# Kernel tuning notes

Measured on AMD Instinct MI355X. Metric: run time of the kernel, lower is better.

The kernel has to match this reference:

```python
import jax, jax.numpy as jnp
import numpy as np

F_DIM = 32          # phi_feature_dim
P = 128             # preselection_ap (spatial H=W)
NU = 4              # num_users
N1 = NU - 1         # n_cat1 == n_cat2
N3 = (NU - 1) ** 2  # n_cat3


def setup_inputs() -> dict:
    key = jax.random.key(0)
    k1, k2, k3, k4, k5 = jax.random.split(key, 5)
    B, CIN = 32, 8
    phi_input = jax.random.normal(k1, (B, CIN, P, P), dtype=jnp.float32)
    W1 = jax.random.normal(k2, (4 * F_DIM, CIN), dtype=jnp.float32) * 0.1
    b1 = jax.random.normal(k3, (4 * F_DIM,), dtype=jnp.float32) * 0.1
    W3 = jax.random.normal(k4, (4 * F_DIM, 4 * F_DIM), dtype=jnp.float32) * 0.1
    b3 = jax.random.normal(k5, (4 * F_DIM,), dtype=jnp.float32) * 0.1
    ex = jnp.ones((P, P), dtype=jnp.float32) - jnp.eye(P, dtype=jnp.float32)
    return {"phi_input": phi_input, "W1": W1, "b1": b1, "W3": W3, "b3": b3, "ex": ex}


def _conv1x1(x, W, b):
    # 1x1 conv == channel matmul: [b,c,h,w] x [o,c] -> [b,o,h,w]
    return jnp.einsum('bchw,oc->bohw', x, W) + b[None, :, None, None]


def _postprocess(r, ex):
    f = F_DIM
    c0 = r[:, :f]
    c1 = jnp.einsum('ph,bchw->bcpw', ex, r[:, f:2 * f]) / N1
    c2 = jnp.einsum('bchw,wq->bchq', r[:, 2 * f:3 * f], ex) / N1
    c3 = jnp.einsum('ph,bchw,wq->bcpq', ex, r[:, 3 * f:4 * f], ex) / N3
    return jnp.concatenate((c0, c1, c2, c3), axis=1)


def reference(phi_input, W1, b1, W3, b3, ex):
    r = jax.nn.relu(_conv1x1(phi_input, W1, b1))
    r = _postprocess(r, ex)
    r = jax.nn.relu(_conv1x1(r, W3, b3))
    r = _postprocess(r, ex)
    return r
```

## Files before the change

### kernel.cpp

```cpp
#include <hip/hip_runtime.h>
#include <stdint.h>

#define BATCH 32
#define CIN   8
#define NCH   128
#define PP    128
#define VCH   96
#define NSTRIP 8

typedef __attribute__((ext_vector_type(8))) short    bf16x8;
typedef __attribute__((ext_vector_type(4))) float    f32x4;

__device__ __forceinline__ float bf2f(unsigned short u) {
    union { unsigned int i; float f; } x; x.i = ((unsigned int)u) << 16; return x.f;
}
__device__ __forceinline__ unsigned short f2bf(float f) {
    union { float f; unsigned int i; } x; x.f = f;
    unsigned int r = x.i + 0x7fffu + ((x.i >> 16) & 1u);
    return (unsigned short)(r >> 16);
}
__device__ __forceinline__ unsigned int pk2(float a, float b) {
    return (unsigned int)f2bf(a) | ((unsigned int)f2bf(b) << 16);
}

#define SWZB(row, cb) (((row) << 8) + ((cb) ^ (((row) & 7) << 4)))

__global__ __launch_bounds__(512) void k1_sums(const float* __restrict__ phi,
        const float* __restrict__ W1, const float* __restrict__ b1,
        float* __restrict__ RS1t, float* __restrict__ CS1p) {
    __shared__ float S[17408];
    int bx = blockIdx.x;
    int b = bx >> 3, strip = bx & 7;
    int p0 = strip * 16;
    int tid = threadIdx.x;
    int c = tid & 127, qq = tid >> 7;

    #pragma unroll
    for (int i = 0; i < 8; ++i) {
        int idx = tid + i * 512;
        int pi = idx >> 8, ci = (idx >> 5) & 7, q4 = (idx & 31) * 4;
        float4 v = *(const float4*)(phi + ((size_t)(b * CIN + ci) * PP + p0 + pi) * PP + q4);
        *(float4*)(S + pi * 1024 + ci * 128 + q4) = v;
    }
    float4 w1a = *(const float4*)(W1 + c * 8);
    float4 w1b = *(const float4*)(W1 + c * 8 + 4);
    float b1c = b1[c];
    float cs_acc[32];
    #pragma unroll
    for (int j = 0; j < 32; ++j) cs_acc[j] = 0.f;
    float rsp[16];
    __syncthreads();

    for (int pi = 0; pi < 16; ++pi) {
        float rs = 0.f;
        const float* pb = S + pi * 1024;
        #pragma unroll
        for (int j4 = 0; j4 < 8; ++j4) {
            int q4 = qq * 32 + j4 * 4;
            float4 ph[8];
            #pragma unroll
            for (int ci = 0; ci < 8; ++ci)
                ph[ci] = *(const float4*)(pb + ci * 128 + q4);
            #pragma unroll
            for (int e = 0; e < 4; ++e) {
                float t = b1c;
                t = fmaf(w1a.x, ((const float*)&ph[0])[e], t);
                t = fmaf(w1a.y, ((const float*)&ph[1])[e], t);
                t = fmaf(w1a.z, ((const float*)&ph[2])[e], t);
                t = fmaf(w1a.w, ((const float*)&ph[3])[e], t);
                t = fmaf(w1b.x, ((const float*)&ph[4])[e], t);
                t = fmaf(w1b.y, ((const float*)&ph[5])[e], t);
                t = fmaf(w1b.z, ((const float*)&ph[6])[e], t);
                t = fmaf(w1b.w, ((const float*)&ph[7])[e], t);
                t = fmaxf(t, 0.f);
                cs_acc[j4 * 4 + e] += t;
                rs += t;
            }
        }
        rsp[pi] = rs;
    }
    __syncthreads();
    #pragma unroll
    for (int pi = 0; pi < 16; ++pi) S[pi * 512 + tid] = rsp[pi];
    __syncthreads();
    #pragma unroll
    for (int i = 0; i < 4; ++i) {
        int idx = tid + i * 512;
        int pi = idx >> 7, cc = idx & 127;
        float s = S[pi * 512 + cc] + S[pi * 512 + 128 + cc]
                + S[pi * 512 + 256 + cc] + S[pi * 512 + 384 + cc];
        RS1t[((size_t)b * PP + p0 + pi) * NCH + cc] = s;
    }
    __syncthreads();
    #pragma unroll
    for (int j4 = 0; j4 < 8; ++j4) {
        float4 v = {cs_acc[j4 * 4], cs_acc[j4 * 4 + 1], cs_acc[j4 * 4 + 2], cs_acc[j4 * 4 + 3]};
        *(float4*)(S + c * 132 + qq * 32 + j4 * 4) = v;
    }
    __syncthreads();
    float* dstp = CS1p + (size_t)(b * NSTRIP + strip) * NCH * PP;
    for (int k = tid; k < 16384; k += 512) {
        int cc = k >> 7, q = k & 127;
        dstp[k] = S[cc * 132 + q];
    }
}

__global__ __launch_bounds__(256) void k1b_planes(const float* __restrict__ W3,
        const float* __restrict__ b3, const float* __restrict__ RS1t,
        const float* __restrict__ CS1p, float* __restrict__ Ap,
        float* __restrict__ Bqt, unsigned short* __restrict__ W3bf) {
    int bx = blockIdx.x;
    int b = bx >> 2, og = bx & 3;
    int tid = threadIdx.x;
    __shared__ float cs_g[64][132];
    __shared__ float rs_g[64][132];
    __shared__ float s1_96[32];
    for (int k = tid; k < 64 * 128; k += 256) {
        int r = k >> 7, q = k & 127;
        int ch_c = (r < 32) ? (32 + r) : (64 + r);
        float s = 0.f;
        #pragma unroll
        for (int s8 = 0; s8 < NSTRIP; ++s8)
            s += CS1p[((size_t)(b * NSTRIP + s8) * NCH + ch_c) * PP + q];
        cs_g[r][q] = s;
    }
    for (int k = tid; k < 64 * 128; k += 256) {
        int p = k >> 6, r = k & 63;
        rs_g[r][p] = RS1t[((size_t)b * PP + p) * NCH + 64 + r];
    }
    __syncthreads();
    if (tid < 32) {
        float s = 0.f;
        for (int q = 0; q < 128; ++q) s += cs_g[32 + tid][q];
        s1_96[tid] = s;
    }
    int o = og * 32 + (tid >> 3), qh = tid & 7;
    {
        float wa[64];
        #pragma unroll
        for (int r = 0; r < 64; ++r)
            wa[r] = (r < 32) ? W3[o * NCH + 32 + r] * (1.f / 3.f)
                             : -W3[o * NCH + 64 + r] * (1.f / 9.f);
        #pragma unroll
        for (int j = 0; j < 4; ++j) {
            int q = qh * 16 + j * 4;
            float4 a = {0.f, 0.f, 0.f, 0.f};
            #pragma unroll
            for (int r = 0; r < 64; ++r) {
                float4 cv = *(const float4*)&cs_g[r][q];
                a.x = fmaf(wa[r], cv.x, a.x);
                a.y = fmaf(wa[r], cv.y, a.y);
                a.z = fmaf(wa[r], cv.z, a.z);
                a.w = fmaf(wa[r], cv.w, a.w);
            }
            *(float4*)&Ap[((size_t)b * NCH + o) * PP + q] = a;
        }
    }
    __syncthreads();
    float cc = b3[o];
    #pragma unroll
    for (int r = 0; r < 32; ++r)
        cc = fmaf(W3[o * NCH + 96 + r] * (1.f / 9.f), s1_96[r], cc);
    {
        float wb[64];
        #pragma unroll
        for (int r = 0; r < 64; ++r)
            wb[r] = (r < 32) ? W3[o * NCH + 64 + r] * (1.f / 3.f)
                             : -W3[o * NCH + 64 + r] * (1.f / 9.f);
        #pragma unroll
        for (int j = 0; j < 4; ++j) {
            int p4 = qh * 16 + j * 4;
            float4 a = {0.f, 0.f, 0.f, 0.f};
            #pragma unroll
            for (int r = 0; r < 64; ++r) {
                float4 rv = *(const float4*)&rs_g[r][p4];
                a.x = fmaf(wb[r], rv.x, a.x);
                a.y = fmaf(wb[r], rv.y, a.y);
                a.z = fmaf(wb[r], rv.z, a.z);
                a.w = fmaf(wb[r], rv.w, a.w);
            }
            Bqt[((size_t)b * PP + p4 + 0) * NCH + o] = a.x + cc;
            Bqt[((size_t)b * PP + p4 + 1) * NCH + o] = a.y + cc;
            Bqt[((size_t)b * PP + p4 + 2) * NCH + o] = a.z + cc;
            Bqt[((size_t)b * PP + p4 + 3) * NCH + o] = a.w + cc;
        }
    }
    if (bx == 0) {
        for (int i = 0; i < 16; ++i) {
            int k = tid + i * 256;
            float4 w = *(const float4*)(W3 + k * 4);
            int c0 = (k * 4) & 127;
            float sc = (c0 < 32) ? 1.f : ((c0 < 96) ? (-1.f / 3.f) : (1.f / 9.f));
            unsigned int lo = pk2(w.x * sc, w.y * sc);
            unsigned int hi = pk2(w.z * sc, w.w * sc);
            uint2 u = {lo, hi};
            *(uint2*)(W3bf + k * 4) = u;
        }
    }
}

__global__ __launch_bounds__(512, 4) void k2_mfma(const float* __restrict__ phi,
        const float* __restrict__ W1, const float* __restrict__ b1,
        const unsigned short* __restrict__ W3bf,
        const float* __restrict__ Ap, const float* __restrict__ Bqt,
        float* __restrict__ out, unsigned short* __restrict__ v2) {
    int bx = blockIdx.x;
    int b = bx >> 4, strip = bx & 15;
    int p0 = strip * 8;
    __shared__ unsigned short w3_l[16384];
    __shared__ unsigned short t_l[16384];
    __shared__ unsigned short phi_b[2][1024];
    __shared__ float BC_l[2][128];
    int tid = threadIdx.x;
    int wv = tid >> 6, l = tid & 63, lr = l & 15, lg = l >> 4;

    #pragma unroll
    for (int i = 0; i < 4; ++i) {
        int k = tid + i * 512;
        int o = k >> 4, cb = (k & 15) * 16;
        bf16x8 v = *(const bf16x8*)(W3bf + k * 8);
        *(bf16x8*)((char*)w3_l + SWZB(o, cb)) = v;
    }
    bf16x8 w1fr = {0, 0, 0, 0, 0, 0, 0, 0};
    if (lg == 0) {
        int cc = wv * 16 + lr;
        float4 wa = *(const float4*)(W1 + cc * 8);
        float4 wb = *(const float4*)(W1 + cc * 8 + 4);
        w1fr[0] = (short)f2bf(wa.x); w1fr[1] = (short)f2bf(wa.y);
        w1fr[2] = (short)f2bf(wa.z); w1fr[3] = (short)f2bf(wa.w);
        w1fr[4] = (short)f2bf(wb.x); w1fr[5] = (short)f2bf(wb.y);
        w1fr[6] = (short)f2bf(wb.z); w1fr[7] = (short)f2bf(wb.w);
    }
    int c0 = wv * 16 + lg * 4;
    f32x4 binit = {b1[c0], b1[c0 + 1], b1[c0 + 2], b1[c0 + 3]};
    if (tid < 128) {
        int q = tid;
        bf16x8 pv;
        #pragma unroll
        for (int ci = 0; ci < 8; ++ci)
            pv[ci] = (short)f2bf(phi[((size_t)(b * CIN + ci) * PP + p0) * PP + q]);
        *(bf16x8*)(phi_b[0] + q * 8) = pv;
        BC_l[0][tid] = Bqt[((size_t)b * PP + p0) * NCH + tid];
    }
    __syncthreads();

    for (int r = 0; r < 8; ++r) {
        int cur = r & 1, nxt = cur ^ 1;
        int p = p0 + r;
        float pfv[8]; float bcn = 0.f;
        if (r < 7 && tid < 128) {
            int q = tid;
            #pragma unroll
            for (int ci = 0; ci < 8; ++ci)
                pfv[ci] = phi[((size_t)(b * CIN + ci) * PP + p + 1) * PP + q];
            bcn = Bqt[((size_t)b * PP + p + 1) * NCH + tid];
        }
        const unsigned short* pb = phi_b[cur];
        #pragma unroll
        for (int pt = 0; pt < 8; ++pt) {
            int pix = pt * 16 + lr;
            bf16x8 bfr1 = {0, 0, 0, 0, 0, 0, 0, 0};
            if (lg == 0) bfr1 = *(const bf16x8*)(pb + pix * 8);
            f32x4 a = __builtin_amdgcn_mfma_f32_16x16x32_bf16(w1fr, bfr1, binit, 0, 0, 0);
            uint2 u;
            u.x = pk2(fmaxf(a.x, 0.f), fmaxf(a.y, 0.f));
            u.y = pk2(fmaxf(a.z, 0.f), fmaxf(a.w, 0.f));
            *(uint2*)((char*)t_l + SWZB(pix, c0 * 2)) = u;
        }
        __syncthreads();
        bf16x8 afr[4];
        #pragma unroll
        for (int ks = 0; ks < 4; ++ks)
            afr[ks] = *(const bf16x8*)((char*)t_l + SWZB(wv * 16 + lr, ks * 64 + lg * 16));
        f32x4 acc[8];
        #pragma unroll
        for (int nt = 0; nt < 8; ++nt) {
            int o = nt * 16 + lr;
            f32x4 ap = *(const f32x4*)(Ap + ((size_t)(b * NCH + o)) * PP + wv * 16 + lg * 4);
            acc[nt] = ap + BC_l[cur][o];
        }
        #pragma unroll
        for (int nt = 0; nt < 8; ++nt) {
            int o = nt * 16 + lr;
            bf16x8 bfr[4];
            #pragma unroll
            for (int ks = 0; ks < 4; ++ks)
                bfr[ks] = *(const bf16x8*)((char*)w3_l + SWZB(o, ks * 64 + lg * 16));
            #pragma unroll
            for (int ks = 0; ks < 4; ++ks)
                acc[nt] = __builtin_amdgcn_mfma_f32_16x16x32_bf16(afr[ks], bfr[ks], acc[nt], 0, 0, 0);
        }
        __syncthreads();
        #pragma unroll
        for (int nt = 0; nt < 2; ++nt) {
            int o = nt * 16 + lr;
            f32x4 a = acc[nt];
            f32x4 rr = {fmaxf(a.x, 0.f), fmaxf(a.y, 0.f), fmaxf(a.z, 0.f), fmaxf(a.w, 0.f)};
            *(f32x4*)(out + ((size_t)(b * NCH + o) * PP + p) * PP + wv * 16 + lg * 4) = rr;
        }
        #pragma unroll
        for (int nt = 2; nt < 8; ++nt) {
            int o = nt * 16 + lr;
            f32x4 a = acc[nt];
            uint2 u;
            u.x = pk2(fmaxf(a.x, 0.f), fmaxf(a.y, 0.f));
            u.y = pk2(fmaxf(a.z, 0.f), fmaxf(a.w, 0.f));
            *(uint2*)((char*)t_l + SWZB(o, (wv * 16 + lg * 4) * 2)) = u;
        }
        if (r < 7 && tid < 128) {
            bf16x8 pv;
            #pragma unroll
            for (int ci = 0; ci < 8; ++ci) pv[ci] = (short)f2bf(pfv[ci]);
            *(bf16x8*)(phi_b[nxt] + tid * 8) = pv;
            BC_l[nxt][tid] = bcn;
        }
        __syncthreads();
        #pragma unroll
        for (int i = 0; i < 3; ++i) {
            int k = tid + i * 512;
            int o = 32 + (k >> 4), j = k & 15;
            bf16x8 v = *(const bf16x8*)((char*)t_l + SWZB(o, j * 16));
            *(bf16x8*)(v2 + ((size_t)(b * VCH + (o - 32)) * PP + p) * PP + j * 8) = v;
        }
        __syncthreads();
    }
}

__global__ __launch_bounds__(256) void k3_out(const unsigned short* __restrict__ v2,
        float* __restrict__ out) {
    int bx = blockIdx.x;
    int b = bx / VCH, cr = bx - b * VCH;
    int ch = 32 + cr;
    int g = ch >> 5;
    __shared__ float rsp[128][16];
    __shared__ float csp[16][128];
    __shared__ float rs_l[128], cs_l[128];
    __shared__ float s_sh;
    int tid = threadIdx.x;
    const unsigned short* src = v2 + (size_t)(b * VCH + cr) * (PP * PP);

    int pc = tid >> 4, qc = tid & 15;
    float cs8[8];
    #pragma unroll
    for (int e = 0; e < 8; ++e) cs8[e] = 0.f;
    #pragma unroll
    for (int i = 0; i < 8; ++i) {
        int pr = pc * 8 + i;
        bf16x8 u = *(const bf16x8*)(src + pr * PP + qc * 8);
        float rp = 0.f;
        #pragma unroll
        for (int e = 0; e < 8; ++e) {
            float v = bf2f((unsigned short)u[e]);
            cs8[e] += v;
            rp += v;
        }
        rsp[pr][qc] = rp;
    }
    f32x4 clo = {cs8[0], cs8[1], cs8[2], cs8[3]};
    f32x4 chi = {cs8[4], cs8[5], cs8[6], cs8[7]};
    *(f32x4*)&csp[pc][qc * 8]     = clo;
    *(f32x4*)&csp[pc][qc * 8 + 4] = chi;
    __syncthreads();
    if (tid < 128) {
        f32x4 a  = *(const f32x4*)&rsp[tid][0];
        f32x4 c2 = *(const f32x4*)&rsp[tid][4];
        f32x4 c3 = *(const f32x4*)&rsp[tid][8];
        f32x4 c4 = *(const f32x4*)&rsp[tid][12];
        rs_l[tid] = (a.x + a.y + a.z + a.w) + (c2.x + c2.y + c2.z + c2.w)
                  + (c3.x + c3.y + c3.z + c3.w) + (c4.x + c4.y + c4.z + c4.w);
    } else {
        int q = tid - 128;
        float s = 0.f;
        #pragma unroll
        for (int i = 0; i < 16; ++i) s += csp[i][q];
        cs_l[q] = s;
    }
    __syncthreads();
    if (tid < 64) {
        float s = rs_l[tid] + rs_l[tid + 64];
        #pragma unroll
        for (int off = 32; off > 0; off >>= 1) s += __shfl_down(s, off);
        if (tid == 0) s_sh = s;
    }
    __syncthreads();
    float stot = s_sh;

    float* dst = out + (size_t)(b * NCH + ch) * (PP * PP);
    #pragma unroll
    for (int i = 0; i < 8; ++i) {
        int k = tid + i * 256;
        int pr = k >> 4, q0 = (k & 15) * 8;
        bf16x8 u = *(const bf16x8*)(src + pr * PP + q0);
        float rp = rs_l[pr];
        float o8[8];
        #pragma unroll
        for (int e = 0; e < 8; ++e) {
            float v = bf2f((unsigned short)u[e]);
            float cq = cs_l[q0 + e];
            float r;
            if (g == 1)      r = (cq - v) * (1.f / 3.f);
            else if (g == 2) r = (rp - v) * (1.f / 3.f);
            else             r = (stot - rp - cq + v) * (1.f / 9.f);
            o8[e] = r;
        }
        f32x4 lo = {o8[0], o8[1], o8[2], o8[3]};
        f32x4 hi = {o8[4], o8[5], o8[6], o8[7]};
        *(f32x4*)(dst + pr * PP + q0)     = lo;
        *(f32x4*)(dst + pr * PP + q0 + 4) = hi;
    }
}

extern "C" void kernel_launch(void* const* d_in, const int* in_sizes, int n_in,
                              void* d_out, int out_size, void* d_ws, size_t ws_size,
                              hipStream_t stream) {
    (void)in_sizes; (void)n_in; (void)out_size; (void)ws_size;
    const float* phi = (const float*)d_in[0];
    const float* W1  = (const float*)d_in[1];
    const float* b1  = (const float*)d_in[2];
    const float* W3  = (const float*)d_in[3];
    const float* b3  = (const float*)d_in[4];
    float* out = (float*)d_out;

    char* ws = (char*)d_ws;
    unsigned short* v2 = (unsigned short*)ws;
    size_t off = (size_t)BATCH * VCH * PP * PP * 2;
    float* RS1t = (float*)(ws + off); off += (size_t)BATCH * NCH * PP * 4;
    float* CS1p = (float*)(ws + off); off += (size_t)BATCH * NSTRIP * NCH * PP * 4;
    float* Ap   = (float*)(ws + off); off += (size_t)BATCH * NCH * PP * 4;
    float* Bqt  = (float*)(ws + off); off += (size_t)BATCH * NCH * PP * 4;
    unsigned short* W3bf = (unsigned short*)(ws + off); off += (size_t)NCH * NCH * 2;

    k1_sums<<<BATCH * NSTRIP, 512, 0, stream>>>(phi, W1, b1, RS1t, CS1p);
    k1b_planes<<<BATCH * 4, 256, 0, stream>>>(W3, b3, RS1t, CS1p, Ap, Bqt, W3bf);
    k2_mfma<<<BATCH * 16, 512, 0, stream>>>(phi, W1, b1, W3bf, Ap, Bqt, out, v2);
    k3_out<<<BATCH * VCH, 256, 0, stream>>>(v2, out);
}
```

Before: 207.4 us.

## Recompute second-stage activations instead of storing bf16 intermediate and re-reading it

The second-layer MFMA pass now runs twice. A first pass computes only the row and column sums needed by the second postprocess, and a small kernel reduces the per-strip column partials. A final pass recomputes the activations and writes the finished output directly. This removes the large bf16 v2 intermediate write and read and the separate k3 pass. In exchange the conv and MFMA work is roughly doubled and one more kernel launch is added.

```diff
diff --git a/kernel.cpp b/kernel.cpp
--- a/kernel.cpp
+++ b/kernel.cpp
@@ -5,8 +5,8 @@
 #define CIN   8
 #define NCH   128
 #define PP    128
-#define VCH   96
 #define NSTRIP 8
+#define KSTRIP 16
 
 typedef __attribute__((ext_vector_type(8))) short    bf16x8;
 typedef __attribute__((ext_vector_type(4))) float    f32x4;
@@ -199,11 +199,11 @@
     }
 }
 
-__global__ __launch_bounds__(512, 4) void k2_mfma(const float* __restrict__ phi,
+__global__ __launch_bounds__(512, 4) void k2a_sums(const float* __restrict__ phi,
         const float* __restrict__ W1, const float* __restrict__ b1,
         const unsigned short* __restrict__ W3bf,
         const float* __restrict__ Ap, const float* __restrict__ Bqt,
-        float* __restrict__ out, unsigned short* __restrict__ v2) {
+        float* __restrict__ RSvT, float* __restrict__ CSp) {
     int bx = blockIdx.x;
     int b = bx >> 4, strip = bx & 15;
     int p0 = strip * 8;
@@ -211,8 +211,10 @@
     __shared__ unsigned short t_l[16384];
     __shared__ unsigned short phi_b[2][1024];
     __shared__ float BC_l[2][128];
+    __shared__ float rs_part[8][64];
     int tid = threadIdx.x;
     int wv = tid >> 6, l = tid & 63, lr = l & 15, lg = l >> 4;
+    int q0 = wv * 16 + lg * 4;
 
     #pragma unroll
     for (int i = 0; i < 4; ++i) {
@@ -234,25 +236,27 @@
     int c0 = wv * 16 + lg * 4;
     f32x4 binit = {b1[c0], b1[c0 + 1], b1[c0 + 2], b1[c0 + 3]};
     if (tid < 128) {
-        int q = tid;
         bf16x8 pv;
         #pragma unroll
         for (int ci = 0; ci < 8; ++ci)
-            pv[ci] = (short)f2bf(phi[((size_t)(b * CIN + ci) * PP + p0) * PP + q]);
-        *(bf16x8*)(phi_b[0] + q * 8) = pv;
+            pv[ci] = (short)f2bf(phi[((size_t)(b * CIN + ci) * PP + p0) * PP + tid]);
+        *(bf16x8*)(phi_b[0] + tid * 8) = pv;
         BC_l[0][tid] = Bqt[((size_t)b * PP + p0) * NCH + tid];
     }
     __syncthreads();
+
+    f32x4 cs_acc[4];
+    #pragma unroll
+    for (int i = 0; i < 4; ++i) { f32x4 z = {0.f, 0.f, 0.f, 0.f}; cs_acc[i] = z; }
 
     for (int r = 0; r < 8; ++r) {
         int cur = r & 1, nxt = cur ^ 1;
         int p = p0 + r;
         float pfv[8]; float bcn = 0.f;
         if (r < 7 && tid < 128) {
-            int q = tid;
             #pragma unroll
             for (int ci = 0; ci < 8; ++ci)
-                pfv[ci] = phi[((size_t)(b * CIN + ci) * PP + p + 1) * PP + q];
+                pfv[ci] = phi[((size_t)(b * CIN + ci) * PP + p + 1) * PP + tid];
             bcn = Bqt[((size_t)b * PP + p + 1) * NCH + tid];
         }
         const unsigned short* pb = phi_b[cur];
@@ -272,13 +276,153 @@
         #pragma unroll
         for (int ks = 0; ks < 4; ++ks)
             afr[ks] = *(const bf16x8*)((char*)t_l + SWZB(wv * 16 + lr, ks * 64 + lg * 16));
-        f32x4 acc[8];
-        #pragma unroll
-        for (int nt = 0; nt < 8; ++nt) {
+        #pragma unroll
+        for (int nt = 2; nt < 8; ++nt) {
             int o = nt * 16 + lr;
-            f32x4 ap = *(const f32x4*)(Ap + ((size_t)(b * NCH + o)) * PP + wv * 16 + lg * 4);
-            acc[nt] = ap + BC_l[cur][o];
-        }
+            bf16x8 bfr[4];
+            #pragma unroll
+            for (int ks = 0; ks < 4; ++ks)
+                bfr[ks] = *(const bf16x8*)((char*)w3_l + SWZB(o, ks * 64 + lg * 16));
+            f32x4 ap = *(const f32x4*)(Ap + ((size_t)(b * NCH + o)) * PP + q0);
+            f32x4 acc = ap + BC_l[cur][o];
+            #pragma unroll
+            for (int ks = 0; ks < 4; ++ks)
+                acc = __builtin_amdgcn_mfma_f32_16x16x32_bf16(afr[ks], bfr[ks], acc, 0, 0, 0);
+            f32x4 v = {fmaxf(acc.x, 0.f), fmaxf(acc.y, 0.f), fmaxf(acc.z, 0.f), fmaxf(acc.w, 0.f)};
+            if (nt < 4) cs_acc[nt - 2] += v;
+            else if (nt >= 6) cs_acc[nt - 4] += v;
+            if (nt >= 4) {
+                float rsv = v.x + v.y + v.z + v.w;
+                rsv += __shfl_xor(rsv, 16);
+                rsv += __shfl_xor(rsv, 32);
+                if (lg == 0) rs_part[wv][(nt - 4) * 16 + lr] = rsv;
+            }
+        }
+        if (r < 7 && tid < 128) {
+            bf16x8 pv;
+            #pragma unroll
+            for (int ci = 0; ci < 8; ++ci) pv[ci] = (short)f2bf(pfv[ci]);
+            *(bf16x8*)(phi_b[nxt] + tid * 8) = pv;
+            BC_l[nxt][tid] = bcn;
+        }
+        __syncthreads();
+        if (tid < 64) {
+            float s = 0.f;
+            #pragma unroll
+            for (int w8 = 0; w8 < 8; ++w8) s += rs_part[w8][tid];
+            RSvT[((size_t)(b * PP + p)) * 64 + tid] = s;
+        }
+    }
+    {
+        float* dst = CSp + ((size_t)(b * KSTRIP + strip)) * 64 * PP;
+        *(f32x4*)(dst + (size_t)(lr)      * PP + q0) = cs_acc[0];
+        *(f32x4*)(dst + (size_t)(16 + lr) * PP + q0) = cs_acc[1];
+        *(f32x4*)(dst + (size_t)(32 + lr) * PP + q0) = cs_acc[2];
+        *(f32x4*)(dst + (size_t)(48 + lr) * PP + q0) = cs_acc[3];
+    }
+}
+
+__global__ __launch_bounds__(256) void k2s_reduce(const float* __restrict__ CSp,
+        const float* __restrict__ RSvT, float* __restrict__ CSv,
+        float* __restrict__ Sb) {
+    int b = blockIdx.x, tid = threadIdx.x;
+    for (int k = tid; k < 64 * PP; k += 256) {
+        float s = 0.f;
+        #pragma unroll
+        for (int st = 0; st < KSTRIP; ++st)
+            s += CSp[((size_t)(b * KSTRIP + st)) * 64 * PP + k];
+        CSv[(size_t)b * 64 * PP + k] = s;
+    }
+    if (tid < 32) {
+        float s = 0.f;
+        for (int p = 0; p < PP; ++p) s += RSvT[((size_t)(b * PP + p)) * 64 + 32 + tid];
+        Sb[b * 32 + tid] = s;
+    }
+}
+
+__global__ __launch_bounds__(512, 4) void k2b_out(const float* __restrict__ phi,
+        const float* __restrict__ W1, const float* __restrict__ b1,
+        const unsigned short* __restrict__ W3bf,
+        const float* __restrict__ Ap, const float* __restrict__ Bqt,
+        const float* __restrict__ RSvT, const float* __restrict__ CSv,
+        const float* __restrict__ Sb, float* __restrict__ out) {
+    int bx = blockIdx.x;
+    int b = bx >> 4, strip = bx & 15;
+    int p0 = strip * 8;
+    __shared__ unsigned short w3_l[16384];
+    __shared__ unsigned short t_l[16384];
+    __shared__ unsigned short phi_b[2][1024];
+    __shared__ float BC_l[2][128];
+    __shared__ float rs_l[2][64];
+    __shared__ float S_l[32];
+    int tid = threadIdx.x;
+    int wv = tid >> 6, l = tid & 63, lr = l & 15, lg = l >> 4;
+    int q0 = wv * 16 + lg * 4;
+
+    #pragma unroll
+    for (int i = 0; i < 4; ++i) {
+        int k = tid + i * 512;
+        int o = k >> 4, cb = (k & 15) * 16;
+        bf16x8 v = *(const bf16x8*)(W3bf + k * 8);
+        *(bf16x8*)((char*)w3_l + SWZB(o, cb)) = v;
+    }
+    bf16x8 w1fr = {0, 0, 0, 0, 0, 0, 0, 0};
+    if (lg == 0) {
+        int cc = wv * 16 + lr;
+        float4 wa = *(const float4*)(W1 + cc * 8);
+        float4 wb = *(const float4*)(W1 + cc * 8 + 4);
+        w1fr[0] = (short)f2bf(wa.x); w1fr[1] = (short)f2bf(wa.y);
+        w1fr[2] = (short)f2bf(wa.z); w1fr[3] = (short)f2bf(wa.w);
+        w1fr[4] = (short)f2bf(wb.x); w1fr[5] = (short)f2bf(wb.y);
+        w1fr[6] = (short)f2bf(wb.z); w1fr[7] = (short)f2bf(wb.w);
+    }
+    int c0 = wv * 16 + lg * 4;
+    f32x4 binit = {b1[c0], b1[c0 + 1], b1[c0 + 2], b1[c0 + 3]};
+    if (tid < 128) {
+        bf16x8 pv;
+        #pragma unroll
+        for (int ci = 0; ci < 8; ++ci)
+            pv[ci] = (short)f2bf(phi[((size_t)(b * CIN + ci) * PP + p0) * PP + tid]);
+        *(bf16x8*)(phi_b[0] + tid * 8) = pv;
+        BC_l[0][tid] = Bqt[((size_t)b * PP + p0) * NCH + tid];
+    } else if (tid < 192) {
+        rs_l[0][tid - 128] = RSvT[((size_t)(b * PP + p0)) * 64 + tid - 128];
+    } else if (tid < 224) {
+        S_l[tid - 192] = Sb[b * 32 + tid - 192];
+    }
+    __syncthreads();
+
+    for (int r = 0; r < 8; ++r) {
+        int cur = r & 1, nxt = cur ^ 1;
+        int p = p0 + r;
+        float pfv[8]; float bcn = 0.f; float rsn = 0.f;
+        if (r < 7) {
+            if (tid < 128) {
+                #pragma unroll
+                for (int ci = 0; ci < 8; ++ci)
+                    pfv[ci] = phi[((size_t)(b * CIN + ci) * PP + p + 1) * PP + tid];
+                bcn = Bqt[((size_t)b * PP + p + 1) * NCH + tid];
+            } else if (tid < 192) {
+                rsn = RSvT[((size_t)(b * PP + p + 1)) * 64 + tid - 128];
+            }
+        }
+        const unsigned short* pb = phi_b[cur];
+        #pragma unroll
+        for (int pt = 0; pt < 8; ++pt) {
+            int pix = pt * 16 + lr;
+            bf16x8 bfr1 = {0, 0, 0, 0, 0, 0, 0, 0};
+            if (lg == 0) bfr1 = *(const bf16x8*)(pb + pix * 8);
+            f32x4 a = __builtin_amdgcn_mfma_f32_16x16x32_bf16(w1fr, bfr1, binit, 0, 0, 0);
+            uint2 u;
+            u.x = pk2(fmaxf(a.x, 0.f), fmaxf(a.y, 0.f));
+            u.y = pk2(fmaxf(a.z, 0.f), fmaxf(a.w, 0.f));
+            *(uint2*)((char*)t_l + SWZB(pix, c0 * 2)) = u;
+        }
+        __syncthreads();
+        bf16x8 afr[4];
+        #pragma unroll
+        for (int ks = 0; ks < 4; ++ks)
+            afr[ks] = *(const bf16x8*)((char*)t_l + SWZB(wv * 16 + lr, ks * 64 + lg * 16));
         #pragma unroll
         for (int nt = 0; nt < 8; ++nt) {
             int o = nt * 16 + lr;
@@ -286,127 +430,42 @@
             #pragma unroll
             for (int ks = 0; ks < 4; ++ks)
                 bfr[ks] = *(const bf16x8*)((char*)w3_l + SWZB(o, ks * 64 + lg * 16));
+            f32x4 ap = *(const f32x4*)(Ap + ((size_t)(b * NCH + o)) * PP + q0);
+            f32x4 acc = ap + BC_l[cur][o];
             #pragma unroll
             for (int ks = 0; ks < 4; ++ks)
-                acc[nt] = __builtin_amdgcn_mfma_f32_16x16x32_bf16(afr[ks], bfr[ks], acc[nt], 0, 0, 0);
+                acc = __builtin_amdgcn_mfma_f32_16x16x32_bf16(afr[ks], bfr[ks], acc, 0, 0, 0);
+            f32x4 v = {fmaxf(acc.x, 0.f), fmaxf(acc.y, 0.f), fmaxf(acc.z, 0.f), fmaxf(acc.w, 0.f)};
+            f32x4 o4;
+            if (nt < 2) {
+                o4 = v;
+            } else if (nt < 4) {
+                f32x4 cs = *(const f32x4*)(CSv + ((size_t)b * 64 + (nt - 2) * 16 + lr) * PP + q0);
+                o4 = (cs - v) * (1.f / 3.f);
+            } else if (nt < 6) {
+                float rp = rs_l[cur][(nt - 4) * 16 + lr];
+                o4 = (rp - v) * (1.f / 3.f);
+            } else {
+                int jr = (nt - 4) * 16 + lr;
+                float rp = rs_l[cur][jr];
+                float sj = S_l[jr - 32];
+                f32x4 cs = *(const f32x4*)(CSv + ((size_t)b * 64 + 32 + (nt - 6) * 16 + lr) * PP + q0);
+                o4 = ((sj - rp) - cs + v) * (1.f / 9.f);
+            }
+            *(f32x4*)(out + ((size_t)(b * NCH + o) * PP + p) * PP + q0) = o4;
+        }
+        if (r < 7) {
+            if (tid < 128) {
+                bf16x8 pv;
+                #pragma unroll
+                for (int ci = 0; ci < 8; ++ci) pv[ci] = (short)f2bf(pfv[ci]);
+                *(bf16x8*)(phi_b[nxt] + tid * 8) = pv;
+                BC_l[nxt][tid] = bcn;
+            } else if (tid < 192) {
+                rs_l[nxt][tid - 128] = rsn;
+            }
         }
         __syncthreads();
-        #pragma unroll
-        for (int nt = 0; nt < 2; ++nt) {
-            int o = nt * 16 + lr;
-            f32x4 a = acc[nt];
-            f32x4 rr = {fmaxf(a.x, 0.f), fmaxf(a.y, 0.f), fmaxf(a.z, 0.f), fmaxf(a.w, 0.f)};
-            *(f32x4*)(out + ((size_t)(b * NCH + o) * PP + p) * PP + wv * 16 + lg * 4) = rr;
-        }
-        #pragma unroll
-        for (int nt = 2; nt < 8; ++nt) {
-            int o = nt * 16 + lr;
-            f32x4 a = acc[nt];
-            uint2 u;
-            u.x = pk2(fmaxf(a.x, 0.f), fmaxf(a.y, 0.f));
-            u.y = pk2(fmaxf(a.z, 0.f), fmaxf(a.w, 0.f));
-            *(uint2*)((char*)t_l + SWZB(o, (wv * 16 + lg * 4) * 2)) = u;
-        }
-        if (r < 7 && tid < 128) {
-            bf16x8 pv;
-            #pragma unroll
-            for (int ci = 0; ci < 8; ++ci) pv[ci] = (short)f2bf(pfv[ci]);
-            *(bf16x8*)(phi_b[nxt] + tid * 8) = pv;
-            BC_l[nxt][tid] = bcn;
-        }
-        __syncthreads();
-        #pragma unroll
-        for (int i = 0; i < 3; ++i) {
-            int k = tid + i * 512;
-            int o = 32 + (k >> 4), j = k & 15;
-            bf16x8 v = *(const bf16x8*)((char*)t_l + SWZB(o, j * 16));
-            *(bf16x8*)(v2 + ((size_t)(b * VCH + (o - 32)) * PP + p) * PP + j * 8) = v;
-        }
-        __syncthreads();
-    }
-}
-
-__global__ __launch_bounds__(256) void k3_out(const unsigned short* __restrict__ v2,
-        float* __restrict__ out) {
-    int bx = blockIdx.x;
-    int b = bx / VCH, cr = bx - b * VCH;
-    int ch = 32 + cr;
-    int g = ch >> 5;
-    __shared__ float rsp[128][16];
-    __shared__ float csp[16][128];
-    __shared__ float rs_l[128], cs_l[128];
-    __shared__ float s_sh;
-    int tid = threadIdx.x;
-    const unsigned short* src = v2 + (size_t)(b * VCH + cr) * (PP * PP);
-
-    int pc = tid >> 4, qc = tid & 15;
-    float cs8[8];
-    #pragma unroll
-    for (int e = 0; e < 8; ++e) cs8[e] = 0.f;
-    #pragma unroll
-    for (int i = 0; i < 8; ++i) {
-        int pr = pc * 8 + i;
-        bf16x8 u = *(const bf16x8*)(src + pr * PP + qc * 8);
-        float rp = 0.f;
-        #pragma unroll
-        for (int e = 0; e < 8; ++e) {
-            float v = bf2f((unsigned short)u[e]);
-            cs8[e] += v;
-            rp += v;
-        }
-        rsp[pr][qc] = rp;
-    }
-    f32x4 clo = {cs8[0], cs8[1], cs8[2], cs8[3]};
-    f32x4 chi = {cs8[4], cs8[5], cs8[6], cs8[7]};
-    *(f32x4*)&csp[pc][qc * 8]     = clo;
-    *(f32x4*)&csp[pc][qc * 8 + 4] = chi;
-    __syncthreads();
-    if (tid < 128) {
-        f32x4 a  = *(const f32x4*)&rsp[tid][0];
-        f32x4 c2 = *(const f32x4*)&rsp[tid][4];
-        f32x4 c3 = *(const f32x4*)&rsp[tid][8];
-        f32x4 c4 = *(const f32x4*)&rsp[tid][12];
-        rs_l[tid] = (a.x + a.y + a.z + a.w) + (c2.x + c2.y + c2.z + c2.w)
-                  + (c3.x + c3.y + c3.z + c3.w) + (c4.x + c4.y + c4.z + c4.w);
-    } else {
-        int q = tid - 128;
-        float s = 0.f;
-        #pragma unroll
-        for (int i = 0; i < 16; ++i) s += csp[i][q];
-        cs_l[q] = s;
-    }
-    __syncthreads();
-    if (tid < 64) {
-        float s = rs_l[tid] + rs_l[tid + 64];
-        #pragma unroll
-        for (int off = 32; off > 0; off >>= 1) s += __shfl_down(s, off);
-        if (tid == 0) s_sh = s;
-    }
-    __syncthreads();
-    float stot = s_sh;
-
-    float* dst = out + (size_t)(b * NCH + ch) * (PP * PP);
-    #pragma unroll
-    for (int i = 0; i < 8; ++i) {
-        int k = tid + i * 256;
-        int pr = k >> 4, q0 = (k & 15) * 8;
-        bf16x8 u = *(const bf16x8*)(src + pr * PP + q0);
-        float rp = rs_l[pr];
-        float o8[8];
-        #pragma unroll
-        for (int e = 0; e < 8; ++e) {
-            float v = bf2f((unsigned short)u[e]);
-            float cq = cs_l[q0 + e];
-            float r;
-            if (g == 1)      r = (cq - v) * (1.f / 3.f);
-            else if (g == 2) r = (rp - v) * (1.f / 3.f);
-            else             r = (stot - rp - cq + v) * (1.f / 9.f);
-            o8[e] = r;
-        }
-        f32x4 lo = {o8[0], o8[1], o8[2], o8[3]};
-        f32x4 hi = {o8[4], o8[5], o8[6], o8[7]};
-        *(f32x4*)(dst + pr * PP + q0)     = lo;
-        *(f32x4*)(dst + pr * PP + q0 + 4) = hi;
     }
 }
 
@@ -422,16 +481,20 @@
     float* out = (float*)d_out;
 
     char* ws = (char*)d_ws;
-    unsigned short* v2 = (unsigned short*)ws;
-    size_t off = (size_t)BATCH * VCH * PP * PP * 2;
+    size_t off = 0;
     float* RS1t = (float*)(ws + off); off += (size_t)BATCH * NCH * PP * 4;
     float* CS1p = (float*)(ws + off); off += (size_t)BATCH * NSTRIP * NCH * PP * 4;
     float* Ap   = (float*)(ws + off); off += (size_t)BATCH * NCH * PP * 4;
     float* Bqt  = (float*)(ws + off); off += (size_t)BATCH * NCH * PP * 4;
     unsigned short* W3bf = (unsigned short*)(ws + off); off += (size_t)NCH * NCH * 2;
+    float* RSvT = (float*)(ws + off); off += (size_t)BATCH * PP * 64 * 4;
+    float* CSp  = (float*)(ws + off); off += (size_t)BATCH * KSTRIP * 64 * PP * 4;
+    float* CSv  = (float*)(ws + off); off += (size_t)BATCH * 64 * PP * 4;
+    float* Sb   = (float*)(ws + off); off += (size_t)BATCH * 32 * 4;
 
     k1_sums<<<BATCH * NSTRIP, 512, 0, stream>>>(phi, W1, b1, RS1t, CS1p);
     k1b_planes<<<BATCH * 4, 256, 0, stream>>>(W3, b3, RS1t, CS1p, Ap, Bqt, W3bf);
-    k2_mfma<<<BATCH * 16, 512, 0, stream>>>(phi, W1, b1, W3bf, Ap, Bqt, out, v2);
-    k3_out<<<BATCH * VCH, 256, 0, stream>>>(v2, out);
-}
+    k2a_sums<<<BATCH * KSTRIP, 512, 0, stream>>>(phi, W1, b1, W3bf, Ap, Bqt, RSvT, CSp);
+    k2s_reduce<<<BATCH, 256, 0, stream>>>(CSp, RSvT, CSv, Sb);
+    k2b_out<<<BATCH * KSTRIP, 512, 0, stream>>>(phi, W1, b1, W3bf, Ap, Bqt, RSvT, CSv, Sb, out);
+}
```

Result: slower. 331.5 us (+59.8%).

## Compute second-layer row/column sums inside MFMA kernel and simplify output pass

Applied to the files above, without the earlier changes.

The MFMA kernel now computes per-channel row sums (through cross-lane shuffles and an LDS partial buffer) and per-strip column sums in registers as it produces the second conv outputs. A small reduce kernel combines the per-strip column sums and the totals, so the final kernel only reads precomputed sums and skips its own reduction pass over v2. In exchange, all 128 channels, including the identity group, are now staged through bf16 v2 instead of c0 being written straight to fp32 output. That adds an extra write and read of that group, rounds it to bf16, and adds one kernel launch.

```diff
diff --git a/kernel.cpp b/kernel.cpp
--- a/kernel.cpp
+++ b/kernel.cpp
@@ -5,8 +5,8 @@
 #define CIN   8
 #define NCH   128
 #define PP    128
-#define VCH   96
 #define NSTRIP 8
+#define KSTRIP 16
 
 typedef __attribute__((ext_vector_type(8))) short    bf16x8;
 typedef __attribute__((ext_vector_type(4))) float    f32x4;
@@ -203,7 +203,8 @@
         const float* __restrict__ W1, const float* __restrict__ b1,
         const unsigned short* __restrict__ W3bf,
         const float* __restrict__ Ap, const float* __restrict__ Bqt,
-        float* __restrict__ out, unsigned short* __restrict__ v2) {
+        unsigned short* __restrict__ v2, float* __restrict__ RSvT,
+        float* __restrict__ CSp) {
     int bx = blockIdx.x;
     int b = bx >> 4, strip = bx & 15;
     int p0 = strip * 8;
@@ -211,8 +212,10 @@
     __shared__ unsigned short t_l[16384];
     __shared__ unsigned short phi_b[2][1024];
     __shared__ float BC_l[2][128];
+    __shared__ float rs_part[8][64];
     int tid = threadIdx.x;
     int wv = tid >> 6, l = tid & 63, lr = l & 15, lg = l >> 4;
+    int q0 = wv * 16 + lg * 4;
 
     #pragma unroll
     for (int i = 0; i < 4; ++i) {
@@ -234,25 +237,27 @@
     int c0 = wv * 16 + lg * 4;
     f32x4 binit = {b1[c0], b1[c0 + 1], b1[c0 + 2], b1[c0 + 3]};
     if (tid < 128) {
-        int q = tid;
         bf16x8 pv;
         #pragma unroll
         for (int ci = 0; ci < 8; ++ci)
-            pv[ci] = (short)f2bf(phi[((size_t)(b * CIN + ci) * PP + p0) * PP + q]);
-        *(bf16x8*)(phi_b[0] + q * 8) = pv;
+            pv[ci] = (short)f2bf(phi[((size_t)(b * CIN + ci) * PP + p0) * PP + tid]);
+        *(bf16x8*)(phi_b[0] + tid * 8) = pv;
         BC_l[0][tid] = Bqt[((size_t)b * PP + p0) * NCH + tid];
     }
     __syncthreads();
+
+    f32x4 cs_acc[4];
+    #pragma unroll
+    for (int i = 0; i < 4; ++i) { f32x4 z = {0.f, 0.f, 0.f, 0.f}; cs_acc[i] = z; }
 
     for (int r = 0; r < 8; ++r) {
         int cur = r & 1, nxt = cur ^ 1;
         int p = p0 + r;
         float pfv[8]; float bcn = 0.f;
         if (r < 7 && tid < 128) {
-            int q = tid;
             #pragma unroll
             for (int ci = 0; ci < 8; ++ci)
-                pfv[ci] = phi[((size_t)(b * CIN + ci) * PP + p + 1) * PP + q];
+                pfv[ci] = phi[((size_t)(b * CIN + ci) * PP + p + 1) * PP + tid];
             bcn = Bqt[((size_t)b * PP + p + 1) * NCH + tid];
         }
         const unsigned short* pb = phi_b[cur];
@@ -272,13 +277,7 @@
         #pragma unroll
         for (int ks = 0; ks < 4; ++ks)
             afr[ks] = *(const bf16x8*)((char*)t_l + SWZB(wv * 16 + lr, ks * 64 + lg * 16));
-        f32x4 acc[8];
-        #pragma unroll
-        for (int nt = 0; nt < 8; ++nt) {
-            int o = nt * 16 + lr;
-            f32x4 ap = *(const f32x4*)(Ap + ((size_t)(b * NCH + o)) * PP + wv * 16 + lg * 4);
-            acc[nt] = ap + BC_l[cur][o];
-        }
+        uint2 vpk[8];
         #pragma unroll
         for (int nt = 0; nt < 8; ++nt) {
             int o = nt * 16 + lr;
@@ -286,26 +285,28 @@
             #pragma unroll
             for (int ks = 0; ks < 4; ++ks)
                 bfr[ks] = *(const bf16x8*)((char*)w3_l + SWZB(o, ks * 64 + lg * 16));
+            f32x4 ap = *(const f32x4*)(Ap + ((size_t)(b * NCH + o)) * PP + q0);
+            f32x4 acc = ap + BC_l[cur][o];
             #pragma unroll
             for (int ks = 0; ks < 4; ++ks)
-                acc[nt] = __builtin_amdgcn_mfma_f32_16x16x32_bf16(afr[ks], bfr[ks], acc[nt], 0, 0, 0);
+                acc = __builtin_amdgcn_mfma_f32_16x16x32_bf16(afr[ks], bfr[ks], acc, 0, 0, 0);
+            f32x4 v = {fmaxf(acc.x, 0.f), fmaxf(acc.y, 0.f), fmaxf(acc.z, 0.f), fmaxf(acc.w, 0.f)};
+            if (nt == 2 || nt == 3) cs_acc[nt - 2] += v;
+            else if (nt >= 6)       cs_acc[nt - 4] += v;
+            if (nt >= 4) {
+                float rsv = v.x + v.y + v.z + v.w;
+                rsv += __shfl_xor(rsv, 16);
+                rsv += __shfl_xor(rsv, 32);
+                if (lg == 0) rs_part[wv][(nt - 4) * 16 + lr] = rsv;
+            }
+            vpk[nt].x = pk2(v.x, v.y);
+            vpk[nt].y = pk2(v.z, v.w);
         }
         __syncthreads();
         #pragma unroll
-        for (int nt = 0; nt < 2; ++nt) {
+        for (int nt = 0; nt < 8; ++nt) {
             int o = nt * 16 + lr;
-            f32x4 a = acc[nt];
-            f32x4 rr = {fmaxf(a.x, 0.f), fmaxf(a.y, 0.f), fmaxf(a.z, 0.f), fmaxf(a.w, 0.f)};
-            *(f32x4*)(out + ((size_t)(b * NCH + o) * PP + p) * PP + wv * 16 + lg * 4) = rr;
-        }
-        #pragma unroll
-        for (int nt = 2; nt < 8; ++nt) {
-            int o = nt * 16 + lr;
-            f32x4 a = acc[nt];
-            uint2 u;
-            u.x = pk2(fmaxf(a.x, 0.f), fmaxf(a.y, 0.f));
-            u.y = pk2(fmaxf(a.z, 0.f), fmaxf(a.w, 0.f));
-            *(uint2*)((char*)t_l + SWZB(o, (wv * 16 + lg * 4) * 2)) = u;
+            *(uint2*)((char*)t_l + SWZB(o, q0 * 2)) = vpk[nt];
         }
         if (r < 7 && tid < 128) {
             bf16x8 pv;
@@ -316,91 +317,80 @@
         }
         __syncthreads();
         #pragma unroll
-        for (int i = 0; i < 3; ++i) {
+        for (int i = 0; i < 4; ++i) {
             int k = tid + i * 512;
-            int o = 32 + (k >> 4), j = k & 15;
+            int o = k >> 4, j = k & 15;
             bf16x8 v = *(const bf16x8*)((char*)t_l + SWZB(o, j * 16));
-            *(bf16x8*)(v2 + ((size_t)(b * VCH + (o - 32)) * PP + p) * PP + j * 8) = v;
+            *(bf16x8*)(v2 + ((size_t)(b * NCH + o) * PP + p) * PP + j * 8) = v;
+        }
+        if (tid < 64) {
+            float s = 0.f;
+            #pragma unroll
+            for (int w8 = 0; w8 < 8; ++w8) s += rs_part[w8][tid];
+            RSvT[((size_t)(b * PP + p)) * 64 + tid] = s;
         }
         __syncthreads();
     }
+    {
+        float* dst = CSp + ((size_t)(b * KSTRIP + strip)) * 64 * PP;
+        *(f32x4*)(dst + (size_t)(lr)      * PP + q0) = cs_acc[0];
+        *(f32x4*)(dst + (size_t)(16 + lr) * PP + q0) = cs_acc[1];
+        *(f32x4*)(dst + (size_t)(32 + lr) * PP + q0) = cs_acc[2];
+        *(f32x4*)(dst + (size_t)(48 + lr) * PP + q0) = cs_acc[3];
+    }
+}
+
+__global__ __launch_bounds__(256) void k2s_reduce(const float* __restrict__ CSp,
+        const float* __restrict__ RSvT, float* __restrict__ CSv,
+        float* __restrict__ Sb) {
+    int b = blockIdx.x, tid = threadIdx.x;
+    for (int k = tid; k < 64 * PP; k += 256) {
+        float s = 0.f;
+        #pragma unroll
+        for (int st = 0; st < KSTRIP; ++st)
+            s += CSp[((size_t)(b * KSTRIP + st)) * 64 * PP + k];
+        CSv[(size_t)b * 64 * PP + k] = s;
+    }
+    if (tid < 32) {
+        float s = 0.f;
+        for (int p = 0; p < PP; ++p) s += RSvT[((size_t)(b * PP + p)) * 64 + 32 + tid];
+        Sb[b * 32 + tid] = s;
+    }
 }
 
 __global__ __launch_bounds__(256) void k3_out(const unsigned short* __restrict__ v2,
-        float* __restrict__ out) {
+        const float* __restrict__ RSvT, const float* __restrict__ CSv,
+        const float* __restrict__ Sb, float* __restrict__ out) {
     int bx = blockIdx.x;
-    int b = bx / VCH, cr = bx - b * VCH;
-    int ch = 32 + cr;
+    int b = bx >> 7, ch = bx & 127;
     int g = ch >> 5;
-    __shared__ float rsp[128][16];
-    __shared__ float csp[16][128];
     __shared__ float rs_l[128], cs_l[128];
-    __shared__ float s_sh;
     int tid = threadIdx.x;
-    const unsigned short* src = v2 + (size_t)(b * VCH + cr) * (PP * PP);
-
-    int pc = tid >> 4, qc = tid & 15;
-    float cs8[8];
-    #pragma unroll
-    for (int e = 0; e < 8; ++e) cs8[e] = 0.f;
-    #pragma unroll
-    for (int i = 0; i < 8; ++i) {
-        int pr = pc * 8 + i;
-        bf16x8 u = *(const bf16x8*)(src + pr * PP + qc * 8);
-        float rp = 0.f;
-        #pragma unroll
-        for (int e = 0; e < 8; ++e) {
-            float v = bf2f((unsigned short)u[e]);
-            cs8[e] += v;
-            rp += v;
-        }
-        rsp[pr][qc] = rp;
-    }
-    f32x4 clo = {cs8[0], cs8[1], cs8[2], cs8[3]};
-    f32x4 chi = {cs8[4], cs8[5], cs8[6], cs8[7]};
-    *(f32x4*)&csp[pc][qc * 8]     = clo;
-    *(f32x4*)&csp[pc][qc * 8 + 4] = chi;
-    __syncthreads();
+    size_t base = (size_t)(b * NCH + ch) * (PP * PP);
+    const unsigned short* src = v2 + base;
+    float* dst = out + base;
     if (tid < 128) {
-        f32x4 a  = *(const f32x4*)&rsp[tid][0];
-        f32x4 c2 = *(const f32x4*)&rsp[tid][4];
-        f32x4 c3 = *(const f32x4*)&rsp[tid][8];
-        f32x4 c4 = *(const f32x4*)&rsp[tid][12];
-        rs_l[tid] = (a.x + a.y + a.z + a.w) + (c2.x + c2.y + c2.z + c2.w)
-                  + (c3.x + c3.y + c3.z + c3.w) + (c4.x + c4.y + c4.z + c4.w);
-    } else {
-        int q = tid - 128;
-        float s = 0.f;
-        #pragma unroll
-        for (int i = 0; i < 16; ++i) s += csp[i][q];
-        cs_l[q] = s;
-    }
-    __syncthreads();
-    if (tid < 64) {
-        float s = rs_l[tid] + rs_l[tid + 64];
-        #pragma unroll
-        for (int off = 32; off > 0; off >>= 1) s += __shfl_down(s, off);
-        if (tid == 0) s_sh = s;
-    }
-    __syncthreads();
-    float stot = s_sh;
-
-    float* dst = out + (size_t)(b * NCH + ch) * (PP * PP);
+        if (g >= 2) rs_l[tid] = RSvT[((size_t)(b * PP) + tid) * 64 + (ch - 64)];
+        if (g == 1) cs_l[tid] = CSv[((size_t)b * 64 + (ch - 32)) * PP + tid];
+        if (g == 3) cs_l[tid] = CSv[((size_t)b * 64 + (ch - 64)) * PP + tid];
+    }
+    float stot = (g == 3) ? Sb[b * 32 + (ch - 96)] : 0.f;
+    __syncthreads();
     #pragma unroll
     for (int i = 0; i < 8; ++i) {
         int k = tid + i * 256;
         int pr = k >> 4, q0 = (k & 15) * 8;
         bf16x8 u = *(const bf16x8*)(src + pr * PP + q0);
-        float rp = rs_l[pr];
+        float rp = (g >= 2) ? rs_l[pr] : 0.f;
         float o8[8];
         #pragma unroll
         for (int e = 0; e < 8; ++e) {
             float v = bf2f((unsigned short)u[e]);
-            float cq = cs_l[q0 + e];
             float r;
-            if (g == 1)      r = (cq - v) * (1.f / 3.f);
+            if (g == 0)      r = v;
+            else if (g == 1) r = (cs_l[q0 + e] - v) * (1.f / 3.f);
             else if (g == 2) r = (rp - v) * (1.f / 3.f);
-            else             r = (stot - rp - cq + v) * (1.f / 9.f);
+            else             r = ((stot - rp) - cs_l[q0 + e] + v) * (1.f / 9.f);
             o8[e] = r;
         }
         f32x4 lo = {o8[0], o8[1], o8[2], o8[3]};
@@ -422,16 +412,21 @@
     float* out = (float*)d_out;
 
     char* ws = (char*)d_ws;
-    unsigned short* v2 = (unsigned short*)ws;
-    size_t off = (size_t)BATCH * VCH * PP * PP * 2;
+    size_t off = 0;
+    unsigned short* v2 = (unsigned short*)(ws + off); off += (size_t)BATCH * NCH * PP * PP * 2;
     float* RS1t = (float*)(ws + off); off += (size_t)BATCH * NCH * PP * 4;
     float* CS1p = (float*)(ws + off); off += (size_t)BATCH * NSTRIP * NCH * PP * 4;
     float* Ap   = (float*)(ws + off); off += (size_t)BATCH * NCH * PP * 4;
     float* Bqt  = (float*)(ws + off); off += (size_t)BATCH * NCH * PP * 4;
     unsigned short* W3bf = (unsigned short*)(ws + off); off += (size_t)NCH * NCH * 2;
+    float* RSvT = (float*)(ws + off); off += (size_t)BATCH * PP * 64 * 4;
+    float* CSp  = (float*)(ws + off); off += (size_t)BATCH * KSTRIP * 64 * PP * 4;
+    float* CSv  = (float*)(ws + off); off += (size_t)BATCH * 64 * PP * 4;
+    float* Sb   = (float*)(ws + off); off += (size_t)BATCH * 32 * 4;
 
     k1_sums<<<BATCH * NSTRIP, 512, 0, stream>>>(phi, W1, b1, RS1t, CS1p);
     k1b_planes<<<BATCH * 4, 256, 0, stream>>>(W3, b3, RS1t, CS1p, Ap, Bqt, W3bf);
-    k2_mfma<<<BATCH * 16, 512, 0, stream>>>(phi, W1, b1, W3bf, Ap, Bqt, out, v2);
-    k3_out<<<BATCH * VCH, 256, 0, stream>>>(v2, out);
-}
+    k2_mfma<<<BATCH * KSTRIP, 512, 0, stream>>>(phi, W1, b1, W3bf, Ap, Bqt, v2, RSvT, CSp);
+    k2s_reduce<<<BATCH, 256, 0, stream>>>(CSp, RSvT, CSv, Sb);
+    k3_out<<<BATCH * NCH, 256, 0, stream>>>(v2, RSvT, CSv, Sb, out);
+}
```

After: 319.8 us. +54.1%, slower.
